# Performance work log

Measured on AMD Instinct MI355X. Metric: run time of the kernel, lower is better.

## Reference

```python
import jax, jax.numpy as jnp
import numpy as np

EPS = 1e-8
ALPHA = 0.05          # params.alpha
K_STEPS = 10          # params.K
MB, C, M, N = 2, 3, 256, 256
P, KS = 32, 7         # n_filters, kernel_size
FKS = 5               # degradation filter size


def _corr(x, w, groups):
    # cross-correlation, SAME zero padding (odd kernels)
    pad = w.shape[-1] // 2
    return jax.lax.conv_general_dilated(
        x, w, (1, 1), [(pad, pad), (pad, pad)],
        dimension_numbers=('NCHW', 'OIHW', 'NCHW'),
        feature_group_count=groups)


def conv_fil(x, fil):
    # depthwise blur: util.conv(x, fil)
    c = x.shape[1]
    w = jnp.broadcast_to(fil, (c, 1) + fil.shape)
    return _corr(x, w, c)


def convT_fil(x, fil):
    # adjoint of conv_fil = correlation with flipped kernel
    return conv_fil(x, fil[::-1, ::-1])


def conv_CSC(a, B):
    # out[b,c] = sum_p corr(a[b,p,c], B[p,c]);  a: (mb,P,C,M,N)
    mb, p, c, m, n = a.shape
    x = a.transpose(0, 2, 1, 3, 4).reshape(mb, c * p, m, n)
    w = B.transpose(1, 0, 2, 3)  # (C, P, k, k), grouped over C
    return _corr(x, w, c)


def convT_CSC(r, B):
    # adjoint: out[b,p,c] = corr(r[b,c], flip(B[p,c]))
    mb, c, m, n = r.shape
    p, k = B.shape[0], B.shape[-1]
    w = B[:, :, ::-1, ::-1].transpose(1, 0, 2, 3).reshape(c * p, 1, k, k)
    y = _corr(r, w, c)
    return y.reshape(mb, c, p, m, n).transpose(0, 2, 1, 3, 4)


def D(x):
    # circular forward differences -> (mb, 2, C, M, N)
    return jnp.stack([jnp.roll(x, -1, axis=-2) - x,
                      jnp.roll(x, -1, axis=-1) - x], axis=1)


def Dt(y):
    # adjoint of D
    y0, y1 = y[:, 0], y[:, 1]
    return (jnp.roll(y0, 1, axis=-2) - y0) + (jnp.roll(y1, 1, axis=-1) - y1)


def soft(x, t):
    return jnp.sign(x) * jnp.maximum(jnp.abs(x) - t, 0.0)


def prox_l12(y, t):
    # group soft-threshold over the 2 gradient components (axis=1)
    nrm = jnp.sqrt(jnp.sum(y * y, axis=1, keepdims=True))
    return y * jnp.maximum(1.0 - t / jnp.maximum(nrm, EPS), 0.0)


def proj_l2ball(v, z, radius):
    # per-sample projection onto {u : ||u - z||_2 <= radius}
    r = v - z
    nrm = jnp.sqrt(jnp.sum(r * r, axis=(1, 2, 3), keepdims=True))
    return z + r * jnp.minimum(1.0, radius / jnp.maximum(nrm, EPS))


def setup_inputs() -> dict:
    key = jax.random.key(0)
    k1, k2, k3 = jax.random.split(key, 3)
    z = jax.random.uniform(k1, (MB, C, M, N), dtype=jnp.float32)
    B = 0.01 * jax.random.normal(k2, (P, C, KS, KS), dtype=jnp.float32)
    a_init = 0.01 * jax.random.normal(k3, (MB, P, C, M, N), dtype=jnp.float32)
    # normalized Gaussian blur (degradation filter)
    g = np.exp(-((np.arange(FKS) - FKS // 2) ** 2) / (2.0 * 1.5 ** 2))
    fil = np.outer(g, g).astype(np.float32)
    fil = jnp.asarray(fil / fil.sum())
    # util.calc_max_singular_P(B[:,0]) via FFT spectral norm of stacked conv ops
    Bh = np.fft.fft2(np.asarray(B[:, 0]), s=(64, 64))
    op_norm = float(np.sqrt(np.max(np.sum(np.abs(Bh) ** 2, axis=0))))
    beta = 1.0 + 2.0 * op_norm + op_norm ** 2
    g1 = 2.0 / beta * 0.9
    g2 = 2.0 / beta * 0.9
    g3 = 1.0 / ((1.0 + 8.0) * 0.9) * (1.0 / g1 - beta / 2.0)
    ones = jnp.ones(K_STEPS, jnp.float32)
    return {'z': z, 'a_init': a_init, 'B': B, 'fil': fil,
            'lam1': 0.01 * ones, 'lam2': 0.01 * ones,
            'gam1': g1 * ones, 'gam2': g2 * ones, 'gam3': g3 * ones}


def reference(z, a_init, B, fil, lam1, lam2, gam1, gam2, gam3):
    mb, c, m, n = z.shape
    epsilon = ALPHA * jnp.sqrt(jnp.float32(c * m * n))
    x0 = convT_fil(z, fil)
    y1_0 = jnp.zeros((mb, 2, c, m, n), z.dtype)
    y2_0 = jnp.zeros_like(z)

    def step(carry, p):
        x_bef, a_bef, y1_bef, y2_bef = carry
        l1, l2, g1, g2, g3 = p
        Ba = conv_CSC(a_bef, B)
        x = x_bef - g1 * (x_bef - Ba + Dt(y1_bef) + convT_fil(y2_bef, fil))
        x_aft = jnp.clip(x, 0.0, 1.0)  # ProxBoxConstraint
        a_aft = soft(a_bef + g2 * convT_CSC(x_bef - Ba, B), g2 * l1)
        v = 2.0 * x_aft - x_bef
        y1 = y1_bef + g3 * D(v)
        y1_aft = y1 - g3 * prox_l12(y1 / (g3 + EPS), l2 / (g3 + EPS))
        y2 = y2_bef + g3 * conv_fil(v, fil)
        y2_aft = y2 - g3 * proj_l2ball(y2 / (g3 + EPS), z, epsilon)
        return (x_aft, a_aft, y1_aft, y2_aft), None

    steps = jnp.stack([lam1, lam2, gam1, gam2, gam3], axis=1)  # (K,5)
    (x_fin, _, _, _), _ = jax.lax.scan(step, (x0, a_init, y1_0, y2_0), steps)
    return x_fin
```

## Files before the change

### kernel.cpp

```cpp
#include <hip/hip_runtime.h>

#define MBn 2
#define Cn 3
#define Mn 256
#define Nn 256
#define Pn 32
#define IMG   65536
#define CIMG  196608
#define XSZ   393216
#define ASZ   12582912
#define EPSf  1e-8f
#define NSTEP 10

#define HW 38
#define HP 40
#define HSZ (HW * HW)

__global__ __launch_bounds__(256) void k_x0(const float* __restrict__ z, const float* __restrict__ fil,
                                            float* __restrict__ x0, float* __restrict__ x0c) {
    int idx = blockIdx.x * 256 + threadIdx.x;
    if (idx >= XSZ) return;
    int j = idx & 255, i = (idx >> 8) & 255, cm = idx >> 16;
    const float* zc = z + cm * IMG;
    float acc = 0.f;
    #pragma unroll
    for (int u = 0; u < 5; ++u) {
        int ii = i + 2 - u;
        if ((unsigned)ii >= (unsigned)Mn) continue;
        #pragma unroll
        for (int v = 0; v < 5; ++v) {
            int jj = j + 2 - v;
            if ((unsigned)jj >= (unsigned)Nn) continue;
            acc += fil[u * 5 + v] * zc[ii * Nn + jj];
        }
    }
    x0[idx] = acc;
    x0c[idx] = acc;
}

__global__ __launch_bounds__(256) void k_convCSC(const float* __restrict__ a, const float* __restrict__ Bg,
                                                 float* __restrict__ Bap) {
    __shared__ float buf[2][HW * HP];
    int blk = blockIdx.x;
    int pg   = blk & 3;
    int tile = (blk >> 2) & 63;
    int cm   = blk >> 8;
    int c = cm % Cn, mb = cm / Cn;
    int i0 = (tile >> 3) * 32, j0 = (tile & 7) * 32;
    int tid = threadIdx.x;
    int tx = tid & 15, ty = tid >> 4;

    int ldsoff[6]; int goff[6]; bool val[6]; bool wm[6];
    #pragma unroll
    for (int k = 0; k < 6; ++k) {
        int l = tid + 256 * k;
        int r = l / HW, cc = l - r * HW;
        int gi = i0 + r - 3, gj = j0 + cc - 3;
        wm[k]  = (l < HSZ);
        val[k] = wm[k] && ((unsigned)gi < (unsigned)Mn) && ((unsigned)gj < (unsigned)Nn);
        ldsoff[k] = r * HP + cc;
        goff[k]   = gi * Nn + gj;
    }

    const float* abase = a + ((size_t)(mb * Pn + pg * 8) * Cn + c) * IMG;
    float rv[6];
    #pragma unroll
    for (int k = 0; k < 6; ++k) rv[k] = val[k] ? abase[goff[k]] : 0.f;

    float acc00 = 0.f, acc01 = 0.f, acc10 = 0.f, acc11 = 0.f;

    for (int pi = 0; pi < 8; ++pi) {
        float* bufc = buf[pi & 1];
        #pragma unroll
        for (int k = 0; k < 6; ++k) if (wm[k]) bufc[ldsoff[k]] = rv[k];
        if (pi < 7) {
            const float* apn = abase + (size_t)(pi + 1) * (Cn * IMG);
            #pragma unroll
            for (int k = 0; k < 6; ++k) rv[k] = val[k] ? apn[goff[k]] : 0.f;
        }
        __syncthreads();
        const float* bp = Bg + ((pg * 8 + pi) * Cn + c) * 49;
        float bv[49];
        #pragma unroll
        for (int k = 0; k < 49; ++k) bv[k] = bp[k];
        #pragma unroll
        for (int r = 0; r < 8; ++r) {
            float w[8];
            const float* rowp = bufc + (2 * ty + r) * HP + 2 * tx;
            #pragma unroll
            for (int k = 0; k < 4; ++k) {
                float2 t = *(const float2*)(rowp + 2 * k);
                w[2 * k] = t.x; w[2 * k + 1] = t.y;
            }
            if (r <= 6) {
                #pragma unroll
                for (int v = 0; v < 7; ++v) {
                    float b = bv[r * 7 + v];
                    acc00 += w[v]     * b;
                    acc01 += w[v + 1] * b;
                }
            }
            if (r >= 1) {
                #pragma unroll
                for (int v = 0; v < 7; ++v) {
                    float b = bv[(r - 1) * 7 + v];
                    acc10 += w[v]     * b;
                    acc11 += w[v + 1] * b;
                }
            }
        }
    }
    float* out = Bap + pg * XSZ + cm * IMG;
    int oi = i0 + 2 * ty, oj = j0 + 2 * tx;
    { float2 st; st.x = acc00; st.y = acc01; *(float2*)(out + oi * Nn + oj) = st; }
    { float2 st; st.x = acc10; st.y = acc11; *(float2*)(out + (oi + 1) * Nn + oj) = st; }
}

__global__ __launch_bounds__(256) void k_xup(const float* __restrict__ xb, const float* __restrict__ Bap,
                                             const float* __restrict__ y1, const float* __restrict__ y2T,
                                             const float* __restrict__ x0c, const float* __restrict__ fil,
                                             const float* __restrict__ gam1, const float* __restrict__ gam3,
                                             const float* __restrict__ scale2, int step,
                                             float* __restrict__ xa, float* __restrict__ rr,
                                             float* __restrict__ vv) {
    int idx = blockIdx.x * 256 + threadIdx.x;
    if (idx >= XSZ) return;
    float g1 = gam1[step];
    int j = idx & 255, i = (idx >> 8) & 255, cm = idx >> 16;
    int mb = cm / Cn, c = cm - mb * Cn;

    float A = 0.f, Bz = 0.f;
    if (step > 0) {
        float g3p = gam3[step - 1];
        float invp = 1.f / (g3p + EPSf);
        float sc = scale2[mb];
        A  = 1.f - g3p * invp * sc;
        Bz = -g3p * (1.f - sc);
    }

    const float* y10 = y1 + (mb * 2) * CIMG + c * IMG;
    const float* y11 = y10 + CIMG;
    int im1 = (i == 0) ? Mn - 1 : i - 1;
    int jm1 = (j == 0) ? Nn - 1 : j - 1;
    float dt = y10[im1 * Nn + j] - y10[i * Nn + j] + y11[i * Nn + jm1] - y11[i * Nn + j];

    const float* Tc = y2T + cm * IMG;
    float cf = 0.f;
    #pragma unroll
    for (int u = 0; u < 5; ++u) {
        int ii = i + 2 - u;
        if ((unsigned)ii >= (unsigned)Mn) continue;
        #pragma unroll
        for (int v = 0; v < 5; ++v) {
            int jj = j + 2 - v;
            if ((unsigned)jj >= (unsigned)Nn) continue;
            cf += fil[u * 5 + v] * Tc[ii * Nn + jj];
        }
    }
    cf = A * cf + Bz * x0c[idx];

    float bav = Bap[idx] + Bap[XSZ + idx] + Bap[2 * XSZ + idx] + Bap[3 * XSZ + idx];
    float xv = xb[idx];
    float xn = xv - g1 * (xv - bav + dt + cf);
    xn = fminf(fmaxf(xn, 0.f), 1.f);
    xa[idx] = xn;
    rr[idx] = xv - bav;
    vv[idx] = 2.f * xn - xv;
}

__global__ __launch_bounds__(256) void k_aup(float* __restrict__ a, const float* __restrict__ rr,
                                             const float* __restrict__ Bg,
                                             const float* __restrict__ lam1, const float* __restrict__ gam2,
                                             int step) {
    __shared__ float rs[HW * HP];
    int blk = blockIdx.x;
    int pg   = blk & 3;
    int tile = (blk >> 2) & 63;
    int cm   = blk >> 8;
    int c = cm % Cn, mb = cm / Cn;
    int i0 = (tile >> 3) * 32, j0 = (tile & 7) * 32;
    int tx = threadIdx.x & 15, ty = threadIdx.x >> 4;

    const float* rp = rr + cm * IMG;
    for (int l = threadIdx.x; l < HSZ; l += 256) {
        int r = l / HW, cc = l - r * HW;
        int gi = i0 + r - 3, gj = j0 + cc - 3;
        float vv = 0.f;
        if ((unsigned)gi < (unsigned)Mn && (unsigned)gj < (unsigned)Nn) vv = rp[gi * Nn + gj];
        rs[r * HP + cc] = vv;
    }
    __syncthreads();

    float w[64];
    #pragma unroll
    for (int r = 0; r < 8; ++r) {
        const float* rowp = rs + (2 * ty + r) * HP + 2 * tx;
        #pragma unroll
        for (int k = 0; k < 4; ++k) {
            float2 t = *(const float2*)(rowp + 2 * k);
            w[r * 8 + 2 * k] = t.x; w[r * 8 + 2 * k + 1] = t.y;
        }
    }

    float g2 = gam2[step], thr = g2 * lam1[step];
    int oi = i0 + 2 * ty, oj = j0 + 2 * tx;

    for (int pi = 0; pi < 8; ++pi) {
        int p = pg * 8 + pi;
        const float* bp = Bg + (p * Cn + c) * 49;
        float bv[49];
        #pragma unroll
        for (int k = 0; k < 49; ++k) bv[k] = bp[k];

        float a00 = 0.f, a01 = 0.f, a10 = 0.f, a11 = 0.f;
        #pragma unroll
        for (int u = 0; u < 7; ++u) {
            #pragma unroll
            for (int v = 0; v < 7; ++v) {
                float b = bv[(6 - u) * 7 + (6 - v)];
                a00 += w[u * 8 + v]           * b;
                a01 += w[u * 8 + v + 1]       * b;
                a10 += w[(u + 1) * 8 + v]     * b;
                a11 += w[(u + 1) * 8 + v + 1] * b;
            }
        }
        float* apo = a + ((size_t)(mb * Pn + p) * Cn + c) * IMG;
        {
            float2 av = *(float2*)(apo + oi * Nn + oj);
            av.x += g2 * a00; av.y += g2 * a01;
            av.x = copysignf(fmaxf(fabsf(av.x) - thr, 0.f), av.x);
            av.y = copysignf(fmaxf(fabsf(av.y) - thr, 0.f), av.y);
            *(float2*)(apo + oi * Nn + oj) = av;
        }
        {
            float2 av = *(float2*)(apo + (oi + 1) * Nn + oj);
            av.x += g2 * a10; av.y += g2 * a11;
            av.x = copysignf(fmaxf(fabsf(av.x) - thr, 0.f), av.x);
            av.y = copysignf(fmaxf(fabsf(av.y) - thr, 0.f), av.y);
            *(float2*)(apo + (oi + 1) * Nn + oj) = av;
        }
    }
}

__global__ __launch_bounds__(256) void k_y12(float* __restrict__ y1, float* __restrict__ y2T,
                                             const float* __restrict__ vv, const float* __restrict__ fil,
                                             const float* __restrict__ z,
                                             const float* __restrict__ lam2, const float* __restrict__ gam3,
                                             const float* __restrict__ scale2, int step,
                                             float* __restrict__ partial) {
    __shared__ float red[256];
    int tid = threadIdx.x;
    int idx = blockIdx.x * 256 + tid;
    float g3 = gam3[step], l2v = lam2[step];
    int j = idx & 255, i = (idx >> 8) & 255, cm = idx >> 16;
    int mb = cm / Cn, c = cm - mb * Cn;
    const float* vc = vv + cm * IMG;

    float A = 0.f, Bz = 0.f;
    if (step > 0) {
        float g3p = gam3[step - 1];
        float invp = 1.f / (g3p + EPSf);
        float sc = scale2[mb];
        A  = 1.f - g3p * invp * sc;
        Bz = -g3p * (1.f - sc);
    }

    int ip1 = (i == Mn - 1) ? 0 : i + 1;
    int jp1 = (j == Nn - 1) ? 0 : j + 1;
    float vij = vc[i * Nn + j];
    float d0 = vc[ip1 * Nn + j] - vij;
    float d1 = vc[i * Nn + jp1] - vij;
    float* y10 = y1 + (mb * 2) * CIMG + c * IMG + i * Nn + j;
    float* y11 = y10 + CIMG;
    float t0 = *y10 + g3 * d0;
    float t1 = *y11 + g3 * d1;
    float inv = 1.f / (g3 + EPSf);
    float w0 = t0 * inv, w1 = t1 * inv;
    float nrm = sqrtf(w0 * w0 + w1 * w1);
    float fac = fmaxf(1.f - (l2v * inv) / fmaxf(nrm, EPSf), 0.f);
    *y10 = t0 - g3 * (w0 * fac);
    *y11 = t1 - g3 * (w1 * fac);

    float cf = 0.f;
    #pragma unroll
    for (int u = 0; u < 5; ++u) {
        int ii2 = i + u - 2;
        if ((unsigned)ii2 >= (unsigned)Mn) continue;
        #pragma unroll
        for (int v = 0; v < 5; ++v) {
            int jj2 = j + v - 2;
            if ((unsigned)jj2 >= (unsigned)Nn) continue;
            cf += fil[u * 5 + v] * vc[ii2 * Nn + jj2];
        }
    }
    float zv = z[idx];
    float t = A * y2T[idx] + Bz * zv + g3 * cf;
    y2T[idx] = t;
    float d = t * inv - zv;
    red[tid] = d * d;
    __syncthreads();
    #pragma unroll
    for (int s = 128; s > 0; s >>= 1) {
        if (tid < s) red[tid] += red[tid + s];
        __syncthreads();
    }
    if (tid == 0) partial[blockIdx.x] = red[0];
}

__global__ __launch_bounds__(256) void k_norm(const float* __restrict__ partial, float* __restrict__ scale2) {
    __shared__ float red[256];
    int tid = threadIdx.x;
    float s = 0.f;
    for (int l = tid; l < 768; l += 256) s += partial[blockIdx.x * 768 + l];
    red[tid] = s;
    __syncthreads();
    #pragma unroll
    for (int k = 128; k > 0; k >>= 1) {
        if (tid < k) red[tid] += red[tid + k];
        __syncthreads();
    }
    if (tid == 0) {
        float nrm = sqrtf(red[0]);
        float radius = 0.05f * sqrtf((float)CIMG);
        scale2[blockIdx.x] = fminf(1.f, radius / fmaxf(nrm, EPSf));
    }
}

extern "C" void kernel_launch(void* const* d_in, const int* in_sizes, int n_in,
                              void* d_out, int out_size, void* d_ws, size_t ws_size,
                              hipStream_t stream) {
    const float* z      = (const float*)d_in[0];
    const float* a_init = (const float*)d_in[1];
    const float* B      = (const float*)d_in[2];
    const float* fil    = (const float*)d_in[3];
    const float* lam1   = (const float*)d_in[4];
    const float* lam2   = (const float*)d_in[5];
    const float* gam1   = (const float*)d_in[6];
    const float* gam2   = (const float*)d_in[7];
    const float* gam3   = (const float*)d_in[8];

    float* ws = (float*)d_ws;
    float* a      = ws;
    float* xA     = a + ASZ;
    float* xB     = xA + XSZ;
    float* x0c    = xB + XSZ;
    float* Bap    = x0c + XSZ;
    float* rr     = Bap + 4 * XSZ;
    float* vv     = rr + XSZ;
    float* y1     = vv + XSZ;
    float* y2T    = y1 + 2 * XSZ;
    float* part   = y2T + XSZ;
    float* scale2 = part + 1536;

    hipMemcpyAsync(a, a_init, (size_t)ASZ * sizeof(float), hipMemcpyDeviceToDevice, stream);
    hipMemsetAsync(y1, 0, (size_t)2 * XSZ * sizeof(float), stream);
    k_x0<<<XSZ / 256, 256, 0, stream>>>(z, fil, xA, x0c);

    float* xin = xA;
    float* xout = xB;
    for (int s = 0; s < NSTEP; ++s) {
        k_convCSC<<<1536, 256, 0, stream>>>(a, B, Bap);
        k_xup<<<XSZ / 256, 256, 0, stream>>>(xin, Bap, y1, y2T, x0c, fil, gam1, gam3, scale2, s,
                                             xout, rr, vv);
        k_aup<<<1536, 256, 0, stream>>>(a, rr, B, lam1, gam2, s);
        k_y12<<<XSZ / 256, 256, 0, stream>>>(y1, y2T, vv, fil, z, lam2, gam3, scale2, s, part);
        k_norm<<<2, 256, 0, stream>>>(part, scale2);
        float* t = xin; xin = xout; xout = t;
    }

    hipMemcpyAsync(d_out, xin, (size_t)XSZ * sizeof(float), hipMemcpyDeviceToDevice, stream);
}
```

Measured before the change: 834.9 us.

## Merge per-step kernels, split conv over more p-groups, drop initial coefficient copy

```diff
diff --git a/kernel.cpp b/kernel.cpp
--- a/kernel.cpp
+++ b/kernel.cpp
@@ -16,6 +16,9 @@
 #define HP 40
 #define HSZ (HW * HW)
 
+#define NCONV 3072
+#define NAUP  1536
+
 __global__ __launch_bounds__(256) void k_x0(const float* __restrict__ z, const float* __restrict__ fil,
                                             float* __restrict__ x0, float* __restrict__ x0c) {
     int idx = blockIdx.x * 256 + threadIdx.x;
@@ -38,16 +41,38 @@
     x0c[idx] = acc;
 }
 
-__global__ __launch_bounds__(256) void k_convCSC(const float* __restrict__ a, const float* __restrict__ Bg,
-                                                 float* __restrict__ Bap) {
+__global__ __launch_bounds__(256) void k_conv(const float* __restrict__ a_in, const float* __restrict__ Bg,
+                                              float* __restrict__ Bap,
+                                              const float* __restrict__ part, float* __restrict__ scale2) {
     __shared__ float buf[2][HW * HP];
     int blk = blockIdx.x;
-    int pg   = blk & 3;
-    int tile = (blk >> 2) & 63;
-    int cm   = blk >> 8;
+    int tid = threadIdx.x;
+
+    if (blk >= NCONV) {
+        float* red = buf[0];
+        int mbi = blk - NCONV;
+        float s = 0.f;
+        for (int l = tid; l < 768; l += 256) s += part[mbi * 768 + l];
+        red[tid] = s;
+        __syncthreads();
+        #pragma unroll
+        for (int k = 128; k > 0; k >>= 1) {
+            if (tid < k) red[tid] += red[tid + k];
+            __syncthreads();
+        }
+        if (tid == 0) {
+            float nrm = sqrtf(red[0]);
+            float radius = 0.05f * sqrtf((float)CIMG);
+            scale2[mbi] = fminf(1.f, radius / fmaxf(nrm, EPSf));
+        }
+        return;
+    }
+
+    int pg   = blk & 7;
+    int tile = (blk >> 3) & 63;
+    int cm   = blk >> 9;
     int c = cm % Cn, mb = cm / Cn;
     int i0 = (tile >> 3) * 32, j0 = (tile & 7) * 32;
-    int tid = threadIdx.x;
     int tx = tid & 15, ty = tid >> 4;
 
     int ldsoff[6]; int goff[6]; bool val[6]; bool wm[6];
@@ -62,24 +87,24 @@
         goff[k]   = gi * Nn + gj;
     }
 
-    const float* abase = a + ((size_t)(mb * Pn + pg * 8) * Cn + c) * IMG;
+    const float* abase = a_in + ((size_t)(mb * Pn + pg * 4) * Cn + c) * IMG;
     float rv[6];
     #pragma unroll
     for (int k = 0; k < 6; ++k) rv[k] = val[k] ? abase[goff[k]] : 0.f;
 
     float acc00 = 0.f, acc01 = 0.f, acc10 = 0.f, acc11 = 0.f;
 
-    for (int pi = 0; pi < 8; ++pi) {
+    for (int pi = 0; pi < 4; ++pi) {
         float* bufc = buf[pi & 1];
         #pragma unroll
         for (int k = 0; k < 6; ++k) if (wm[k]) bufc[ldsoff[k]] = rv[k];
-        if (pi < 7) {
+        if (pi < 3) {
             const float* apn = abase + (size_t)(pi + 1) * (Cn * IMG);
             #pragma unroll
             for (int k = 0; k < 6; ++k) rv[k] = val[k] ? apn[goff[k]] : 0.f;
         }
         __syncthreads();
-        const float* bp = Bg + ((pg * 8 + pi) * Cn + c) * 49;
+        const float* bp = Bg + ((pg * 4 + pi) * Cn + c) * 49;
         float bv[49];
         #pragma unroll
         for (int k = 0; k < 49; ++k) bv[k] = bp[k];
@@ -159,7 +184,9 @@
     }
     cf = A * cf + Bz * x0c[idx];
 
-    float bav = Bap[idx] + Bap[XSZ + idx] + Bap[2 * XSZ + idx] + Bap[3 * XSZ + idx];
+    float bav = 0.f;
+    #pragma unroll
+    for (int k = 0; k < 8; ++k) bav += Bap[k * XSZ + idx];
     float xv = xb[idx];
     float xn = xv - g1 * (xv - bav + dt + cf);
     xn = fminf(fmaxf(xn, 0.f), 1.f);
@@ -168,161 +195,146 @@
     vv[idx] = 2.f * xn - xv;
 }
 
-__global__ __launch_bounds__(256) void k_aup(float* __restrict__ a, const float* __restrict__ rr,
-                                             const float* __restrict__ Bg,
-                                             const float* __restrict__ lam1, const float* __restrict__ gam2,
-                                             int step) {
-    __shared__ float rs[HW * HP];
+__global__ __launch_bounds__(256) void k_ay(const float* __restrict__ a_in, float* __restrict__ a_out,
+                                            const float* __restrict__ rr, const float* __restrict__ Bg,
+                                            float* __restrict__ y1, float* __restrict__ y2T,
+                                            const float* __restrict__ vv, const float* __restrict__ fil,
+                                            const float* __restrict__ z,
+                                            const float* __restrict__ lam1, const float* __restrict__ lam2,
+                                            const float* __restrict__ gam2, const float* __restrict__ gam3,
+                                            const float* __restrict__ scale2, int step,
+                                            float* __restrict__ partial) {
+    __shared__ float sh[HW * HP];
     int blk = blockIdx.x;
-    int pg   = blk & 3;
-    int tile = (blk >> 2) & 63;
-    int cm   = blk >> 8;
-    int c = cm % Cn, mb = cm / Cn;
-    int i0 = (tile >> 3) * 32, j0 = (tile & 7) * 32;
-    int tx = threadIdx.x & 15, ty = threadIdx.x >> 4;
-
-    const float* rp = rr + cm * IMG;
-    for (int l = threadIdx.x; l < HSZ; l += 256) {
-        int r = l / HW, cc = l - r * HW;
-        int gi = i0 + r - 3, gj = j0 + cc - 3;
-        float vv = 0.f;
-        if ((unsigned)gi < (unsigned)Mn && (unsigned)gj < (unsigned)Nn) vv = rp[gi * Nn + gj];
-        rs[r * HP + cc] = vv;
-    }
-    __syncthreads();
-
-    float w[64];
-    #pragma unroll
-    for (int r = 0; r < 8; ++r) {
-        const float* rowp = rs + (2 * ty + r) * HP + 2 * tx;
-        #pragma unroll
-        for (int k = 0; k < 4; ++k) {
-            float2 t = *(const float2*)(rowp + 2 * k);
-            w[r * 8 + 2 * k] = t.x; w[r * 8 + 2 * k + 1] = t.y;
-        }
-    }
-
-    float g2 = gam2[step], thr = g2 * lam1[step];
-    int oi = i0 + 2 * ty, oj = j0 + 2 * tx;
-
-    for (int pi = 0; pi < 8; ++pi) {
-        int p = pg * 8 + pi;
-        const float* bp = Bg + (p * Cn + c) * 49;
-        float bv[49];
-        #pragma unroll
-        for (int k = 0; k < 49; ++k) bv[k] = bp[k];
-
-        float a00 = 0.f, a01 = 0.f, a10 = 0.f, a11 = 0.f;
-        #pragma unroll
-        for (int u = 0; u < 7; ++u) {
-            #pragma unroll
-            for (int v = 0; v < 7; ++v) {
-                float b = bv[(6 - u) * 7 + (6 - v)];
-                a00 += w[u * 8 + v]           * b;
-                a01 += w[u * 8 + v + 1]       * b;
-                a10 += w[(u + 1) * 8 + v]     * b;
-                a11 += w[(u + 1) * 8 + v + 1] * b;
-            }
-        }
-        float* apo = a + ((size_t)(mb * Pn + p) * Cn + c) * IMG;
-        {
-            float2 av = *(float2*)(apo + oi * Nn + oj);
-            av.x += g2 * a00; av.y += g2 * a01;
-            av.x = copysignf(fmaxf(fabsf(av.x) - thr, 0.f), av.x);
-            av.y = copysignf(fmaxf(fabsf(av.y) - thr, 0.f), av.y);
-            *(float2*)(apo + oi * Nn + oj) = av;
-        }
-        {
-            float2 av = *(float2*)(apo + (oi + 1) * Nn + oj);
-            av.x += g2 * a10; av.y += g2 * a11;
-            av.x = copysignf(fmaxf(fabsf(av.x) - thr, 0.f), av.x);
-            av.y = copysignf(fmaxf(fabsf(av.y) - thr, 0.f), av.y);
-            *(float2*)(apo + (oi + 1) * Nn + oj) = av;
-        }
-    }
-}
-
-__global__ __launch_bounds__(256) void k_y12(float* __restrict__ y1, float* __restrict__ y2T,
-                                             const float* __restrict__ vv, const float* __restrict__ fil,
-                                             const float* __restrict__ z,
-                                             const float* __restrict__ lam2, const float* __restrict__ gam3,
-                                             const float* __restrict__ scale2, int step,
-                                             float* __restrict__ partial) {
-    __shared__ float red[256];
     int tid = threadIdx.x;
-    int idx = blockIdx.x * 256 + tid;
-    float g3 = gam3[step], l2v = lam2[step];
-    int j = idx & 255, i = (idx >> 8) & 255, cm = idx >> 16;
-    int mb = cm / Cn, c = cm - mb * Cn;
-    const float* vc = vv + cm * IMG;
-
-    float A = 0.f, Bz = 0.f;
-    if (step > 0) {
-        float g3p = gam3[step - 1];
-        float invp = 1.f / (g3p + EPSf);
-        float sc = scale2[mb];
-        A  = 1.f - g3p * invp * sc;
-        Bz = -g3p * (1.f - sc);
-    }
-
-    int ip1 = (i == Mn - 1) ? 0 : i + 1;
-    int jp1 = (j == Nn - 1) ? 0 : j + 1;
-    float vij = vc[i * Nn + j];
-    float d0 = vc[ip1 * Nn + j] - vij;
-    float d1 = vc[i * Nn + jp1] - vij;
-    float* y10 = y1 + (mb * 2) * CIMG + c * IMG + i * Nn + j;
-    float* y11 = y10 + CIMG;
-    float t0 = *y10 + g3 * d0;
-    float t1 = *y11 + g3 * d1;
-    float inv = 1.f / (g3 + EPSf);
-    float w0 = t0 * inv, w1 = t1 * inv;
-    float nrm = sqrtf(w0 * w0 + w1 * w1);
-    float fac = fmaxf(1.f - (l2v * inv) / fmaxf(nrm, EPSf), 0.f);
-    *y10 = t0 - g3 * (w0 * fac);
-    *y11 = t1 - g3 * (w1 * fac);
-
-    float cf = 0.f;
-    #pragma unroll
-    for (int u = 0; u < 5; ++u) {
-        int ii2 = i + u - 2;
-        if ((unsigned)ii2 >= (unsigned)Mn) continue;
-        #pragma unroll
-        for (int v = 0; v < 5; ++v) {
-            int jj2 = j + v - 2;
-            if ((unsigned)jj2 >= (unsigned)Nn) continue;
-            cf += fil[u * 5 + v] * vc[ii2 * Nn + jj2];
-        }
-    }
-    float zv = z[idx];
-    float t = A * y2T[idx] + Bz * zv + g3 * cf;
-    y2T[idx] = t;
-    float d = t * inv - zv;
-    red[tid] = d * d;
-    __syncthreads();
-    #pragma unroll
-    for (int s = 128; s > 0; s >>= 1) {
-        if (tid < s) red[tid] += red[tid + s];
+
+    if (blk < NAUP) {
+        int pg   = blk & 3;
+        int tile = (blk >> 2) & 63;
+        int cm   = blk >> 8;
+        int c = cm % Cn, mb = cm / Cn;
+        int i0 = (tile >> 3) * 32, j0 = (tile & 7) * 32;
+        int tx = tid & 15, ty = tid >> 4;
+
+        const float* rp = rr + cm * IMG;
+        for (int l = tid; l < HSZ; l += 256) {
+            int r = l / HW, cc = l - r * HW;
+            int gi = i0 + r - 3, gj = j0 + cc - 3;
+            float v = 0.f;
+            if ((unsigned)gi < (unsigned)Mn && (unsigned)gj < (unsigned)Nn) v = rp[gi * Nn + gj];
+            sh[r * HP + cc] = v;
+        }
         __syncthreads();
-    }
-    if (tid == 0) partial[blockIdx.x] = red[0];
-}
-
-__global__ __launch_bounds__(256) void k_norm(const float* __restrict__ partial, float* __restrict__ scale2) {
-    __shared__ float red[256];
-    int tid = threadIdx.x;
-    float s = 0.f;
-    for (int l = tid; l < 768; l += 256) s += partial[blockIdx.x * 768 + l];
-    red[tid] = s;
-    __syncthreads();
-    #pragma unroll
-    for (int k = 128; k > 0; k >>= 1) {
-        if (tid < k) red[tid] += red[tid + k];
+
+        float w[64];
+        #pragma unroll
+        for (int r = 0; r < 8; ++r) {
+            const float* rowp = sh + (2 * ty + r) * HP + 2 * tx;
+            #pragma unroll
+            for (int k = 0; k < 4; ++k) {
+                float2 t = *(const float2*)(rowp + 2 * k);
+                w[r * 8 + 2 * k] = t.x; w[r * 8 + 2 * k + 1] = t.y;
+            }
+        }
+
+        float g2 = gam2[step], thr = g2 * lam1[step];
+        int oi = i0 + 2 * ty, oj = j0 + 2 * tx;
+
+        for (int pi = 0; pi < 8; ++pi) {
+            int p = pg * 8 + pi;
+            const float* bp = Bg + (p * Cn + c) * 49;
+            float bv[49];
+            #pragma unroll
+            for (int k = 0; k < 49; ++k) bv[k] = bp[k];
+
+            float a00 = 0.f, a01 = 0.f, a10 = 0.f, a11 = 0.f;
+            #pragma unroll
+            for (int u = 0; u < 7; ++u) {
+                #pragma unroll
+                for (int v = 0; v < 7; ++v) {
+                    float b = bv[(6 - u) * 7 + (6 - v)];
+                    a00 += w[u * 8 + v]           * b;
+                    a01 += w[u * 8 + v + 1]       * b;
+                    a10 += w[(u + 1) * 8 + v]     * b;
+                    a11 += w[(u + 1) * 8 + v + 1] * b;
+                }
+            }
+            size_t base = ((size_t)(mb * Pn + p) * Cn + c) * IMG;
+            {
+                size_t off = base + oi * Nn + oj;
+                float2 av = *(const float2*)(a_in + off);
+                av.x += g2 * a00; av.y += g2 * a01;
+                av.x = copysignf(fmaxf(fabsf(av.x) - thr, 0.f), av.x);
+                av.y = copysignf(fmaxf(fabsf(av.y) - thr, 0.f), av.y);
+                *(float2*)(a_out + off) = av;
+            }
+            {
+                size_t off = base + (size_t)(oi + 1) * Nn + oj;
+                float2 av = *(const float2*)(a_in + off);
+                av.x += g2 * a10; av.y += g2 * a11;
+                av.x = copysignf(fmaxf(fabsf(av.x) - thr, 0.f), av.x);
+                av.y = copysignf(fmaxf(fabsf(av.y) - thr, 0.f), av.y);
+                *(float2*)(a_out + off) = av;
+            }
+        }
+    } else {
+        float* red = sh;
+        int pblk = blk - NAUP;
+        int idx = pblk * 256 + tid;
+        float g3 = gam3[step], l2v = lam2[step];
+        int j = idx & 255, i = (idx >> 8) & 255, cm = idx >> 16;
+        int mb = cm / Cn, c = cm - mb * Cn;
+        const float* vc = vv + cm * IMG;
+
+        float A = 0.f, Bz = 0.f;
+        if (step > 0) {
+            float g3p = gam3[step - 1];
+            float invp = 1.f / (g3p + EPSf);
+            float sc = scale2[mb];
+            A  = 1.f - g3p * invp * sc;
+            Bz = -g3p * (1.f - sc);
+        }
+
+        int ip1 = (i == Mn - 1) ? 0 : i + 1;
+        int jp1 = (j == Nn - 1) ? 0 : j + 1;
+        float vij = vc[i * Nn + j];
+        float d0 = vc[ip1 * Nn + j] - vij;
+        float d1 = vc[i * Nn + jp1] - vij;
+        float* y10 = y1 + (mb * 2) * CIMG + c * IMG + i * Nn + j;
+        float* y11 = y10 + CIMG;
+        float t0 = *y10 + g3 * d0;
+        float t1 = *y11 + g3 * d1;
+        float inv = 1.f / (g3 + EPSf);
+        float w0 = t0 * inv, w1 = t1 * inv;
+        float nrm = sqrtf(w0 * w0 + w1 * w1);
+        float fac = fmaxf(1.f - (l2v * inv) / fmaxf(nrm, EPSf), 0.f);
+        *y10 = t0 - g3 * (w0 * fac);
+        *y11 = t1 - g3 * (w1 * fac);
+
+        float cf = 0.f;
+        #pragma unroll
+        for (int u = 0; u < 5; ++u) {
+            int ii2 = i + u - 2;
+            if ((unsigned)ii2 >= (unsigned)Mn) continue;
+            #pragma unroll
+            for (int v = 0; v < 5; ++v) {
+                int jj2 = j + v - 2;
+                if ((unsigned)jj2 >= (unsigned)Nn) continue;
+                cf += fil[u * 5 + v] * vc[ii2 * Nn + jj2];
+            }
+        }
+        float zv = z[idx];
+        float t = A * y2T[idx] + Bz * zv + g3 * cf;
+        y2T[idx] = t;
+        float d = t * inv - zv;
+        red[tid] = d * d;
         __syncthreads();
-    }
-    if (tid == 0) {
-        float nrm = sqrtf(red[0]);
-        float radius = 0.05f * sqrtf((float)CIMG);
-        scale2[blockIdx.x] = fminf(1.f, radius / fmaxf(nrm, EPSf));
+        #pragma unroll
+        for (int s = 128; s > 0; s >>= 1) {
+            if (tid < s) red[tid] += red[tid + s];
+            __syncthreads();
+        }
+        if (tid == 0) partial[pblk] = red[0];
     }
 }
 
@@ -345,26 +357,25 @@
     float* xB     = xA + XSZ;
     float* x0c    = xB + XSZ;
     float* Bap    = x0c + XSZ;
-    float* rr     = Bap + 4 * XSZ;
+    float* rr     = Bap + 8 * XSZ;
     float* vv     = rr + XSZ;
     float* y1     = vv + XSZ;
     float* y2T    = y1 + 2 * XSZ;
     float* part   = y2T + XSZ;
     float* scale2 = part + 1536;
 
-    hipMemcpyAsync(a, a_init, (size_t)ASZ * sizeof(float), hipMemcpyDeviceToDevice, stream);
     hipMemsetAsync(y1, 0, (size_t)2 * XSZ * sizeof(float), stream);
     k_x0<<<XSZ / 256, 256, 0, stream>>>(z, fil, xA, x0c);
 
     float* xin = xA;
     float* xout = xB;
     for (int s = 0; s < NSTEP; ++s) {
-        k_convCSC<<<1536, 256, 0, stream>>>(a, B, Bap);
+        const float* a_src = (s == 0) ? a_init : a;
+        k_conv<<<NCONV + 2, 256, 0, stream>>>(a_src, B, Bap, part, scale2);
         k_xup<<<XSZ / 256, 256, 0, stream>>>(xin, Bap, y1, y2T, x0c, fil, gam1, gam3, scale2, s,
                                              xout, rr, vv);
-        k_aup<<<1536, 256, 0, stream>>>(a, rr, B, lam1, gam2, s);
-        k_y12<<<XSZ / 256, 256, 0, stream>>>(y1, y2T, vv, fil, z, lam2, gam3, scale2, s, part);
-        k_norm<<<2, 256, 0, stream>>>(part, scale2);
+        k_ay<<<NAUP + 1536, 256, 0, stream>>>(a_src, a, rr, B, y1, y2T, vv, fil, z,
+                                              lam1, lam2, gam2, gam3, scale2, s, part);
         float* t = xin; xin = xout; xout = t;
     }
 
```

New measurement: 1.229 ms. 1.47x slower.
